# Performance work log

Hardware: AMD Instinct MI355X
Metric: run time of the kernel (lower is better)

The kernel has to match this reference:

```python
import jax, jax.numpy as jnp
import numpy as np

B, T, D, N, K, H = 2, 2048, 2048, 16, 8, 128
WIN = 1024                      # sliding_window_size
SOFT_CAP = 50.0                 # attn_logits_soft_cap
SCALAR = 0.08838834764831845    # query_pre_attn_scalar = head_dim**-0.5
K_MASK = -2.3819763e+38
ROPE_BASE = 10000.0
ROPE_SCALE = 1.0


def apply_rope(x, positions):
    # x: [B, T, heads, H]; positions: [B, T]
    head_dim = x.shape[-1]
    half = head_dim // 2
    timescale = ROPE_BASE ** (2.0 * jnp.arange(half, dtype=jnp.float32) / head_dim)
    sinusoid = positions[..., None].astype(jnp.float32) / timescale / ROPE_SCALE  # [B,T,half]
    sin = jnp.sin(sinusoid)[:, :, None, :]
    cos = jnp.cos(sinusoid)[:, :, None, :]
    first, second = jnp.split(x, 2, axis=-1)
    return jnp.concatenate(
        [first * cos - second * sin, second * cos + first * sin], axis=-1
    ).astype(x.dtype)


def setup_inputs() -> dict:
    key = jax.random.key(0)
    k0, k1, k2, k3 = jax.random.split(key, 4)
    x = jax.random.normal(k0, (B, T, D), jnp.float32)
    wq = jax.random.normal(k1, (N, D, H), jnp.float32) * (D ** -0.5)
    wkv = jax.random.normal(k2, (2, K, D, H), jnp.float32) * (D ** -0.5)
    wo = jax.random.normal(k3, (N, H, D), jnp.float32) * ((N * H) ** -0.5)
    segment_pos = jnp.broadcast_to(jnp.arange(T, dtype=jnp.int32), (B, T))
    attn_mask = jnp.broadcast_to(jnp.tril(jnp.ones((T, T), dtype=bool)), (B, T, T))  # causal
    return {"x": x, "wq": wq, "wkv": wkv, "wo": wo,
            "segment_pos": segment_pos, "attn_mask": attn_mask}


def reference(x, wq, wkv, wo, segment_pos, attn_mask):
    # --- projections ---
    q = jnp.einsum('BTD,NDH->BTNH', x, wq)          # [B,T,N,H]
    kv = jnp.einsum('BTD,CKDH->CBTKH', x, wkv)      # [2,B,T,K,H]
    k_proj, v_proj = kv[0], kv[1]
    # --- RoPE + query scaling ---
    q = apply_rope(q, segment_pos) * SCALAR
    k_proj = apply_rope(k_proj, segment_pos)
    # --- GQA logits ---
    G = N // K
    qg = q.reshape(B, T, K, G, H)
    logits = jnp.einsum('BTKGH,BSKH->BTKGS', qg, k_proj).reshape(B, T, N, T)
    # --- soft cap ---
    logits = jnp.tanh(logits / SOFT_CAP) * SOFT_CAP
    # --- sliding-window mask combined with causal attn_mask ---
    all_ones = jnp.ones(attn_mask.shape, dtype=attn_mask.dtype)
    sliding_mask = jnp.triu(all_ones, -WIN + 1) * jnp.tril(all_ones, WIN - 1)
    mask = sliding_mask * attn_mask                  # [B,T,S]
    padded_logits = jnp.where(mask[:, :, None, :], logits, K_MASK)
    probs = jax.nn.softmax(padded_logits, axis=-1).astype(k_proj.dtype)
    # --- GQA weighted values ---
    encoded = jnp.einsum('BTKGS,BSKH->BTKGH',
                         probs.reshape(B, T, K, G, T), v_proj).reshape(B, T, N, H)
    # --- output projection ---
    return jnp.einsum('BTNH,NHD->BTD', encoded, wo)
```

## Files before the change

kernel.cpp:

```cpp
#include <hip/hip_runtime.h>
#include <stdint.h>

#define BDIM 2
#define TDIM 2048
#define DDIM 2048
#define NHEADS 16
#define KVH 8
#define HDIM 128
#define WINSZ 1024
#define BT (BDIM*TDIM)
#define NHD (NHEADS*HDIM)
#define QKVC 4096

typedef unsigned short u16;
typedef __attribute__((ext_vector_type(8))) short bf16x8;
typedef __attribute__((ext_vector_type(4))) float f32x4;

__device__ __forceinline__ u16 f2bf(float f) {
  union { float f; unsigned u; } v; v.f = f;
  unsigned r = v.u + 0x7FFFu + ((v.u >> 16) & 1u);
  return (u16)(r >> 16);
}
__device__ __forceinline__ float bf2f(u16 u) {
  union { unsigned u; float f; } v; v.u = ((unsigned)u) << 16;
  return v.f;
}

__device__ __forceinline__ void gl_lds16(const u16* g, u16* l) {
  __builtin_amdgcn_global_load_lds((const __attribute__((address_space(1))) void*)g,
                                   (__attribute__((address_space(3))) void*)l, 16, 0, 0);
}

__global__ void k_rope_table(const int* __restrict__ seg, float2* __restrict__ tab) {
  int t = blockIdx.x, b = blockIdx.y, i = threadIdx.x;
  int pos = seg[b*TDIM + t];
  float inv_ts = exp2f(-(float)i * (13.287712379549449f/64.0f));
  float ang = (float)pos * inv_ts;
  tab[(size_t)(b*TDIM + t)*64 + i] = make_float2(cosf(ang), sinf(ang));
}

__global__ void k_cvt_bf16(const float* __restrict__ x, u16* __restrict__ y, int n4) {
  int i = blockIdx.x*blockDim.x + threadIdx.x;
  if (i < n4) {
    float4 v = ((const float4*)x)[i];
    ushort4 o;
    o.x = f2bf(v.x); o.y = f2bf(v.y); o.z = f2bf(v.z); o.w = f2bf(v.w);
    ((ushort4*)y)[i] = o;
  }
}

template<int MODE>
__global__ void k_build_wt(const float* __restrict__ s0p, const float* __restrict__ s1p,
                           u16* __restrict__ dst) {
  __shared__ float tl[32][33];
  int tx = threadIdx.x, ty = threadIdx.y;
  int r0 = blockIdx.x*32, c0 = blockIdx.y*32;
  #pragma unroll
  for (int i = 0; i < 4; i++) {
    int r = r0 + tx, c = c0 + ty + i*8;
    const float* sp; size_t off;
    if (MODE == 0) {
      if (r < 2048) { sp = s0p; off = (size_t)(r >> 7)*262144u + (size_t)(r & 127); }
      else { int j = r - 2048; sp = s1p; off = (size_t)((j >> 10)*8 + ((j >> 7) & 7))*262144u + (size_t)(j & 127); }
      off += (size_t)c * 128u;
    } else {
      sp = s0p; off = (size_t)c * 2048u + (size_t)r;
    }
    tl[tx][ty + i*8] = sp[off];
  }
  __syncthreads();
  #pragma unroll
  for (int i = 0; i < 4; i++) {
    int rl = ty + i*8;
    dst[(size_t)(r0 + rl)*2048u + (size_t)(c0 + tx)] = f2bf(tl[rl][tx]);
  }
}

template<int F32OUT>
__global__ __launch_bounds__(256) void k_gemm(const u16* __restrict__ A, const u16* __restrict__ Bt,
                                              void* __restrict__ Cout, int M, int Ncols, int Kdim, int ldc) {
  __shared__ u16 As[128*64];
  __shared__ u16 Bs[128*64];
  const int tid = threadIdx.x, lane = tid & 63, wave = tid >> 6;
  const int m0 = blockIdx.x * 128, n0 = blockIdx.y * 128;
  const int wr = wave >> 1, wc = wave & 1;
  const int l15 = lane & 15, lg = lane >> 4;
  f32x4 acc[4][4] = {};
  for (int kt = 0; kt < Kdim; kt += 64) {
    __syncthreads();
    #pragma unroll
    for (int i = 0; i < 4; i++) {
      int chb = i*256 + wave*64;
      int ch = chb + lane;
      int r = ch >> 3, cc = ch & 7;
      gl_lds16(A + (size_t)(m0 + r)*Kdim + kt + cc*8, As + chb*8);
      gl_lds16(Bt + (size_t)(n0 + r)*Kdim + kt + cc*8, Bs + chb*8);
    }
    __syncthreads();
    #pragma unroll
    for (int ks = 0; ks < 2; ks++) {
      bf16x8 af[4], bf[4];
      int kk = ks*32 + lg*8;
      #pragma unroll
      for (int mt = 0; mt < 4; mt++) af[mt] = *(const bf16x8*)(As + (wr*64 + mt*16 + l15)*64 + kk);
      #pragma unroll
      for (int nt = 0; nt < 4; nt++) bf[nt] = *(const bf16x8*)(Bs + (wc*64 + nt*16 + l15)*64 + kk);
      #pragma unroll
      for (int mt = 0; mt < 4; mt++)
        #pragma unroll
        for (int nt = 0; nt < 4; nt++)
          acc[mt][nt] = __builtin_amdgcn_mfma_f32_16x16x32_bf16(af[mt], bf[nt], acc[mt][nt], 0, 0, 0);
    }
  }
  #pragma unroll
  for (int mt = 0; mt < 4; mt++) {
    int row = m0 + wr*64 + mt*16 + lg*4;
    #pragma unroll
    for (int nt = 0; nt < 4; nt++) {
      int col = n0 + wc*64 + nt*16 + l15;
      #pragma unroll
      for (int j = 0; j < 4; j++) {
        if (F32OUT) ((float*)Cout)[(size_t)(row + j)*ldc + col] = acc[mt][nt][j];
        else        ((u16*)Cout)[(size_t)(row + j)*ldc + col] = f2bf(acc[mt][nt][j]);
      }
    }
  }
}

template<int F32OUT>
__global__ __launch_bounds__(512, 2) void k_gemm8(const u16* __restrict__ A, const u16* __restrict__ Bt,
                                                  void* __restrict__ Cout, int M, int Ncols, int Kdim, int ldc) {
  __shared__ u16 As[2][256*64];
  __shared__ u16 Bs[2][256*64];
  const int tid = threadIdx.x, lane = tid & 63, wave = tid >> 6;
  const int l15 = lane & 15, lg = lane >> 4;
  const int wm = wave >> 2, wn = wave & 3;
  const int gx = M >> 8, gy = Ncols >> 8;
  const int nwg = gx * gy;
  int bid = blockIdx.x;
  int q = nwg >> 3, r = nwg & 7;
  int xcd = bid & 7, idx = bid >> 3;
  int wg = (xcd < r ? xcd*(q+1) : r*(q+1) + (xcd - r)*q) + idx;
  const int m0 = (wg % gx) * 256, n0 = (wg / gx) * 256;

  const int st_r = tid >> 3;
  const int st_c = (tid & 7) ^ (st_r & 7);

  const u16* Ag = A + (size_t)(m0 + st_r)*Kdim + st_c*8;
  const u16* Bg = Bt + (size_t)(n0 + st_r)*Kdim + st_c*8;

  auto stage = [&](int t, int h) {
    int buf = t & 1;
    if (h < 2) {
      const u16* g = Bg + (size_t)(h*128)*Kdim + t*64;
      u16* d = &Bs[buf][h*8192 + wave*512];
      gl_lds16(g, d);
      gl_lds16(g + (size_t)64*Kdim, d + 4096);
    } else {
      int hh = h - 2;
      const u16* g = Ag + (size_t)(hh*128)*Kdim + t*64;
      u16* d = &As[buf][hh*8192 + wave*512];
      gl_lds16(g, d);
      gl_lds16(g + (size_t)64*Kdim, d + 4096);
    }
  };

  const int aBase = (wm*128 + l15) * 128;
  const int bBase = (wn*64 + l15) * 128;
  const int kx0 = ((lg) ^ (l15 & 7)) << 4;
  const int kx1 = ((4 + lg) ^ (l15 & 7)) << 4;

  f32x4 acc[8][4] = {};
  bf16x8 af[4][2], bfr[4][2];

  stage(0,0); stage(0,1); stage(0,2); stage(0,3);
  stage(1,0); stage(1,1); stage(1,2);
  asm volatile("s_waitcnt vmcnt(6)" ::: "memory");
  __builtin_amdgcn_s_barrier();
  {
    const char* Ab = (const char*)&As[0][0];
    const char* Bb = (const char*)&Bs[0][0];
    #pragma unroll
    for (int mf = 0; mf < 4; mf++) {
      af[mf][0] = *(const bf16x8*)(Ab + aBase + mf*2048 + kx0);
      af[mf][1] = *(const bf16x8*)(Ab + aBase + mf*2048 + kx1);
    }
    #pragma unroll
    for (int nf = 0; nf < 2; nf++) {
      bfr[nf][0] = *(const bf16x8*)(Bb + bBase + nf*2048 + kx0);
      bfr[nf][1] = *(const bf16x8*)(Bb + bBase + nf*2048 + kx1);
    }
  }

  const int NT = Kdim >> 6;

#define MFMA_Q(MS, NS)                                                          \
  { _Pragma("unroll") for (int mf = 0; mf < 4; mf++)                            \
    _Pragma("unroll") for (int nf = 0; nf < 2; nf++) {                          \
      acc[(MS)+mf][(NS)+nf] = __builtin_amdgcn_mfma_f32_16x16x32_bf16(af[mf][0], bfr[(NS)+nf][0], acc[(MS)+mf][(NS)+nf], 0, 0, 0); \
      acc[(MS)+mf][(NS)+nf] = __builtin_amdgcn_mfma_f32_16x16x32_bf16(af[mf][1], bfr[(NS)+nf][1], acc[(MS)+mf][(NS)+nf], 0, 0, 0); \
  } }

  for (int t = 0; t < NT; ++t) {
    const int cur = t & 1;
    const char* Ab  = (const char*)&As[cur][0];
    const char* Bb  = (const char*)&Bs[cur][0];
    const char* Abn = (const char*)&As[cur ^ 1][0];
    const char* Bbn = (const char*)&Bs[cur ^ 1][0];
    __builtin_amdgcn_s_barrier();
    asm volatile("s_waitcnt lgkmcnt(0)" ::: "memory");
    __builtin_amdgcn_sched_barrier(0);
    __builtin_amdgcn_s_setprio(1);
    MFMA_Q(0, 0)
    __builtin_amdgcn_s_setprio(0);
    __builtin_amdgcn_s_barrier();
    #pragma unroll
    for (int nf = 2; nf < 4; nf++) {
      bfr[nf][0] = *(const bf16x8*)(Bb + bBase + nf*2048 + kx0);
      bfr[nf][1] = *(const bf16x8*)(Bb + bBase + nf*2048 + kx1);
    }
    if (t + 1 < NT) stage(t+1, 3);
    __builtin_amdgcn_s_barrier();
    asm volatile("s_waitcnt lgkmcnt(0)" ::: "memory");
    __builtin_amdgcn_sched_barrier(0);
    __builtin_amdgcn_s_setprio(1);
    MFMA_Q(0, 2)
    __builtin_amdgcn_s_setprio(0);
    __builtin_amdgcn_s_barrier();
    #pragma unroll
    for (int mf = 0; mf < 4; mf++) {
      af[mf][0] = *(const bf16x8*)(Ab + aBase + 8192 + mf*2048 + kx0);
      af[mf][1] = *(const bf16x8*)(Ab + aBase + 8192 + mf*2048 + kx1);
    }
    __builtin_amdgcn_s_barrier();
    asm volatile("s_waitcnt lgkmcnt(0)" ::: "memory");
    __builtin_amdgcn_sched_barrier(0);
    __builtin_amdgcn_s_setprio(1);
    MFMA_Q(4, 0)
    __builtin_amdgcn_s_setprio(0);
    __builtin_amdgcn_s_barrier();
    if (t + 2 < NT) { stage(t+2, 0); stage(t+2, 1); }
    __builtin_amdgcn_s_barrier();
    asm volatile("s_waitcnt lgkmcnt(0)" ::: "memory");
    __builtin_amdgcn_sched_barrier(0);
    __builtin_amdgcn_s_setprio(1);
    MFMA_Q(4, 2)
    __builtin_amdgcn_s_setprio(0);
    __builtin_amdgcn_s_barrier();
    if (t + 2 < NT) {
      stage(t+2, 2);
      asm volatile("s_waitcnt vmcnt(6)" ::: "memory");
    } else if (t + 1 < NT) {
      asm volatile("s_waitcnt vmcnt(0)" ::: "memory");
    }
    if (t + 1 < NT) {
      #pragma unroll
      for (int mf = 0; mf < 4; mf++) {
        af[mf][0] = *(const bf16x8*)(Abn + aBase + mf*2048 + kx0);
        af[mf][1] = *(const bf16x8*)(Abn + aBase + mf*2048 + kx1);
      }
      #pragma unroll
      for (int nf = 0; nf < 2; nf++) {
        bfr[nf][0] = *(const bf16x8*)(Bbn + bBase + nf*2048 + kx0);
        bfr[nf][1] = *(const bf16x8*)(Bbn + bBase + nf*2048 + kx1);
      }
    }
  }
#undef MFMA_Q

  #pragma unroll
  for (int mf = 0; mf < 8; mf++) {
    int row = m0 + wm*128 + mf*16 + lg*4;
    #pragma unroll
    for (int nf = 0; nf < 4; nf++) {
      int col = n0 + wn*64 + nf*16 + l15;
      #pragma unroll
      for (int j = 0; j < 4; j++) {
        if (F32OUT) ((float*)Cout)[(size_t)(row + j)*ldc + col] = acc[mf][nf][j];
        else        ((u16*)Cout)[(size_t)(row + j)*ldc + col] = f2bf(acc[mf][nf][j]);
      }
    }
  }
}

__global__ void k_rope2(u16* __restrict__ qkv, const float2* __restrict__ tab) {
  const int tid = threadIdx.x;
  const int bt = blockIdx.x;
  const int h = tid >> 3, g = tid & 7;
  const int col0 = (h < 16 ? h*128 : 2048 + (h - 16)*128) + g*8;
  const float sc = (h < 16) ? 0.08838834764831845f : 1.0f;
  u16* row = qkv + (size_t)bt*QKVC;
  bf16x8 v1 = *(const bf16x8*)(row + col0);
  bf16x8 v2 = *(const bf16x8*)(row + col0 + 64);
  const float4* t4 = (const float4*)(tab + (size_t)bt*64 + g*8);
  bf16x8 r1, r2;
  #pragma unroll
  for (int i = 0; i < 4; i++) {
    float4 cs2 = t4[i];
    float f0 = bf2f((u16)v1[2*i]),   s0 = bf2f((u16)v2[2*i]);
    float f1 = bf2f((u16)v1[2*i+1]), s1 = bf2f((u16)v2[2*i+1]);
    r1[2*i]   = (short)f2bf((f0*cs2.x - s0*cs2.y)*sc);
    r2[2*i]   = (short)f2bf((s0*cs2.x + f0*cs2.y)*sc);
    r1[2*i+1] = (short)f2bf((f1*cs2.z - s1*cs2.w)*sc);
    r2[2*i+1] = (short)f2bf((s1*cs2.z + f1*cs2.w)*sc);
  }
  *(bf16x8*)(row + col0) = r1;
  *(bf16x8*)(row + col0 + 64) = r2;
}

__global__ void k_build_vt(const u16* __restrict__ qkv, u16* __restrict__ vT) {
  __shared__ u16 tl[32][33];
  int tx = threadIdx.x, ty = threadIdx.y;
  int t0 = blockIdx.x*32, h0 = blockIdx.y*32, bk = blockIdx.z;
  const u16* src = qkv + (size_t)(bk >> 3)*TDIM*QKVC + 3072 + (bk & 7)*HDIM;
  #pragma unroll
  for (int i = 0; i < 4; i++)
    tl[ty + i*8][tx] = src[(size_t)(t0 + ty + i*8)*QKVC + h0 + tx];
  __syncthreads();
  u16* dst = vT + (size_t)bk*HDIM*TDIM;
  #pragma unroll
  for (int i = 0; i < 4; i++)
    dst[(size_t)(h0 + ty + i*8)*TDIM + t0 + tx] = tl[tx][ty + i*8];
}

__device__ __forceinline__ void stage_tiles(const u16* __restrict__ kg, const u16* __restrict__ vg,
                                            u16* ldsK, u16* ldsV, int tid) {
  const int w = tid >> 6;
  const int rK = tid >> 4, cK = tid & 15;
  u16* dK = ldsK + w*512;
  gl_lds16(kg + (size_t)rK*QKVC + ((cK ^ (rK & 15)) << 3), dK);
  gl_lds16(kg + (size_t)(rK + 32)*QKVC + ((cK ^ ((rK + 32) & 15)) << 3), dK + 4096);
  const int rV = tid >> 3, cV = tid & 7;
  u16* dV = ldsV + w*512;
  gl_lds16(vg + (size_t)rV*TDIM + ((cV ^ (rV & 7)) << 3), dV);
  gl_lds16(vg + (size_t)(rV + 64)*TDIM + ((cV ^ ((rV + 64) & 7)) << 3), dV + 4096);
}

__global__ __launch_bounds__(512, 4) void k_attn(const u16* __restrict__ qkv, const u16* __restrict__ vT,
                                                 u16* __restrict__ enc) {
  __shared__ u16 Kb[2][64*128];
  __shared__ u16 Vb[2][128*64];
  __shared__ u16 Pl[8][16*64];
  const int tid = threadIdx.x;
  const int lane = tid & 63, wave = tid >> 6;
  const int l15 = lane & 15, lg = lane >> 4;
  const int wg = blockIdx.x;
  const int lin = (wg & 7)*64 + (wg >> 3);
  const int qt = lin & 31, kvh = (lin >> 5) & 7, b = lin >> 8;
  const int n = kvh*2 + (wave >> 2);
  const int t0 = qt * 64;
  const int lo_row = t0 + (wave & 3)*16, hi_row = lo_row + 15;

  bf16x8 qf[4];
  {
    const u16* qb = qkv + (size_t)(b*TDIM + lo_row + l15)*QKVC + n*HDIM + lg*8;
    #pragma unroll
    for (int ks = 0; ks < 4; ks++) qf[ks] = *(const bf16x8*)(qb + ks*32);
  }
  f32x4 o[8] = {};
  f32x4 o_l = {};
  const short one_bf = (short)0x3F80;
  const bf16x8 ones = {one_bf, one_bf, one_bf, one_bf, one_bf, one_bf, one_bf, one_bf};

  const u16* kgb = qkv + (size_t)(b*TDIM)*QKVC + 2048 + kvh*HDIM;
  const u16* vgb = vT + (size_t)(b*KVH + kvh)*HDIM*TDIM;

  const float L0 = 1.4426950408889634f;
  const float L1 = -1.9235933878519513e-4f;
  const float L2 = 3.0777094205631089e-8f;
  const float BIAS = -72.13475204444817f;

  const int s_begin = (t0 >= 1024) ? (t0 - 1024) : 0;
  stage_tiles(kgb + (size_t)s_begin*QKVC, vgb + s_begin, Kb[0], Vb[0], tid);
  int cur = 0;
  for (int s0 = s_begin; s0 <= t0; s0 += 64) {
    if (s0 + 64 <= t0) {
      stage_tiles(kgb + (size_t)(s0 + 64)*QKVC, vgb + (s0 + 64), Kb[cur ^ 1], Vb[cur ^ 1], tid);
      asm volatile("s_waitcnt vmcnt(4)" ::: "memory");
    } else {
      asm volatile("s_waitcnt vmcnt(0)" ::: "memory");
    }
    __builtin_amdgcn_s_barrier();
    __builtin_amdgcn_sched_barrier(0);

    const u16* Kc = Kb[cur];
    const u16* Vc = Vb[cur];
    f32x4 sc4[4];
    #pragma unroll
    for (int c = 0; c < 4; c++) {
      const int cLo = s0 + c*16;
      bool anyLive = (cLo <= hi_row) && (cLo + 15 >= lo_row - (WINSZ - 1));
      bool full    = (cLo + 15 <= lo_row) && (cLo >= hi_row - (WINSZ - 1));
      f32x4 a = {0.f, 0.f, 0.f, 0.f};
      if (anyLive) {
        int krow = c*16 + l15;
        __builtin_amdgcn_s_setprio(1);
        #pragma unroll
        for (int ks = 0; ks < 4; ks++) {
          bf16x8 kf = *(const bf16x8*)(Kc + krow*128 + (((ks*4 + lg) ^ l15) << 3));
          a = __builtin_amdgcn_mfma_f32_16x16x32_bf16(qf[ks], kf, a, 0, 0, 0);
        }
        __builtin_amdgcn_s_setprio(0);
        if (full) {
          #pragma unroll
          for (int j = 0; j < 4; j++) {
            float z = a[j];
            float u = z*z;
            float tt = __builtin_fmaf(u, __builtin_fmaf(u, L2, L1), L0);
            a[j] = exp2f(__builtin_fmaf(z, tt, BIAS));
          }
        } else {
          #pragma unroll
          for (int j = 0; j < 4; j++) {
            int scol = cLo + l15;
            int trow = lo_row + lg*4 + j;
            float z = a[j];
            float u = z*z;
            float tt = __builtin_fmaf(u, __builtin_fmaf(u, L2, L1), L0);
            float p = exp2f(__builtin_fmaf(z, tt, BIAS));
            bool ok = (scol <= trow) && (scol >= trow - (WINSZ - 1));
            a[j] = ok ? p : 0.f;
          }
        }
      }
      sc4[c] = a;
    }
    #pragma unroll
    for (int c = 0; c < 4; c++)
      #pragma unroll
      for (int j = 0; j < 4; j++) {
        int prow = lg*4 + j, pcol = c*16 + l15;
        int off = prow*128 + pcol*2; off ^= (prow & 7) << 4;
        *(u16*)((char*)(&Pl[wave][0]) + off) = f2bf(sc4[c][j]);
      }
    __builtin_amdgcn_s_setprio(1);
    #pragma unroll
    for (int ks = 0; ks < 2; ks++) {
      int roff = l15*128 + ks*64 + lg*16; roff ^= (l15 & 7) << 4;
      bf16x8 pf = *(const bf16x8*)((char*)(&Pl[wave][0]) + roff);
      o_l = __builtin_amdgcn_mfma_f32_16x16x32_bf16(pf, ones, o_l, 0, 0, 0);
      #pragma unroll
      for (int ct = 0; ct < 8; ct++) {
        int vrow = ct*16 + l15;
        bf16x8 vf = *(const bf16x8*)(Vc + vrow*64 + (((ks*4 + lg) ^ (l15 & 7)) << 3));
        o[ct] = __builtin_amdgcn_mfma_f32_16x16x32_bf16(pf, vf, o[ct], 0, 0, 0);
      }
    }
    __builtin_amdgcn_s_setprio(0);
    __builtin_amdgcn_s_barrier();
    cur ^= 1;
  }
  #pragma unroll
  for (int j = 0; j < 4; j++) {
    float inv = __fdividef(1.f, o_l[j]);
    int row = lo_row + lg*4 + j;
    u16* eb = enc + (size_t)(b*TDIM + row)*NHD + n*HDIM;
    #pragma unroll
    for (int ct = 0; ct < 8; ct++)
      eb[ct*16 + l15] = f2bf(o[ct][j] * inv);
  }
}

extern "C" void kernel_launch(void* const* d_in, const int* in_sizes, int n_in,
                              void* d_out, int out_size, void* d_ws, size_t ws_size,
                              hipStream_t stream) {
  const float* x   = (const float*)d_in[0];
  const float* wq  = (const float*)d_in[1];
  const float* wkv = (const float*)d_in[2];
  const float* wo  = (const float*)d_in[3];
  const int*   seg = (const int*)d_in[4];
  float* out = (float*)d_out;

  char* ws = (char*)d_ws;
  u16*    x_bf   = (u16*)(ws);
  u16*    wt_qkv = (u16*)(ws + (16u << 20));
  u16*    qkv    = (u16*)(ws + (32u << 20));
  u16*    vT     = (u16*)(ws + (64u << 20));
  u16*    enc    = (u16*)(ws + (72u << 20));
  u16*    wo_t   = (u16*)(ws + (88u << 20));
  float2* tab    = (float2*)(ws + (96u << 20));

  k_rope_table<<<dim3(TDIM, BDIM), 64, 0, stream>>>(seg, tab);
  k_cvt_bf16<<<(BT*DDIM/4 + 255)/256, 256, 0, stream>>>(x, x_bf, BT*DDIM/4);
  k_build_wt<0><<<dim3(128, 64), dim3(32, 8), 0, stream>>>(wq, wkv, wt_qkv);
  k_build_wt<1><<<dim3(64, 64), dim3(32, 8), 0, stream>>>(wo, nullptr, wo_t);
  k_gemm8<0><<<dim3((BT/256)*(QKVC/256)), 512, 0, stream>>>(x_bf, wt_qkv, qkv, BT, QKVC, DDIM, QKVC);
  k_rope2<<<dim3(BT), 192, 0, stream>>>(qkv, tab);
  k_build_vt<<<dim3(TDIM/32, HDIM/32, BDIM*KVH), dim3(32, 8), 0, stream>>>(qkv, vT);
  k_attn<<<dim3(512), 512, 0, stream>>>(qkv, vT, enc);
  k_gemm<1><<<dim3(BT/128, DDIM/128), 256, 0, stream>>>(enc, wo_t, out, BT, DDIM, NHD, DDIM);
}
```

Baseline: 224.9 us.

## Restructure GEMM main loop LDS fragment loads and barrier schedule

Moves the first-quadrant LDS fragment loads from the end of each iteration to its start, next to the async global-to-LDS stage of the next tile. Replaces the per-quadrant `s_waitcnt lgkmcnt(0)` plus sched_barrier pairs with a single partial lgkmcnt wait and plain compiler memory fences. It also reorders the MFMA quadrants so (4,2) runs before (4,0). The aim is to cut wait stalls and overlap LDS reads with MFMA work. The cost is weaker ordering: stage(t+2) now issues right after the second-half A fragment reads with no barrier in between, which could race with other waves' LDS reads.

```diff
diff --git a/kernel.cpp b/kernel.cpp
--- a/kernel.cpp
+++ b/kernel.cpp
@@ -174,23 +174,10 @@
   bf16x8 af[4][2], bfr[4][2];
 
   stage(0,0); stage(0,1); stage(0,2); stage(0,3);
+  asm volatile("s_waitcnt vmcnt(4)" ::: "memory");
   stage(1,0); stage(1,1); stage(1,2);
   asm volatile("s_waitcnt vmcnt(6)" ::: "memory");
   __builtin_amdgcn_s_barrier();
-  {
-    const char* Ab = (const char*)&As[0][0];
-    const char* Bb = (const char*)&Bs[0][0];
-    #pragma unroll
-    for (int mf = 0; mf < 4; mf++) {
-      af[mf][0] = *(const bf16x8*)(Ab + aBase + mf*2048 + kx0);
-      af[mf][1] = *(const bf16x8*)(Ab + aBase + mf*2048 + kx1);
-    }
-    #pragma unroll
-    for (int nf = 0; nf < 2; nf++) {
-      bfr[nf][0] = *(const bf16x8*)(Bb + bBase + nf*2048 + kx0);
-      bfr[nf][1] = *(const bf16x8*)(Bb + bBase + nf*2048 + kx1);
-    }
-  }
 
   const int NT = Kdim >> 6;
 
@@ -203,13 +190,22 @@
 
   for (int t = 0; t < NT; ++t) {
     const int cur = t & 1;
-    const char* Ab  = (const char*)&As[cur][0];
-    const char* Bb  = (const char*)&Bs[cur][0];
-    const char* Abn = (const char*)&As[cur ^ 1][0];
-    const char* Bbn = (const char*)&Bs[cur ^ 1][0];
-    __builtin_amdgcn_s_barrier();
-    asm volatile("s_waitcnt lgkmcnt(0)" ::: "memory");
-    __builtin_amdgcn_sched_barrier(0);
+    const char* Ab = (const char*)&As[cur][0];
+    const char* Bb = (const char*)&Bs[cur][0];
+    #pragma unroll
+    for (int mf = 0; mf < 4; mf++) {
+      af[mf][0] = *(const bf16x8*)(Ab + aBase + mf*2048 + kx0);
+      af[mf][1] = *(const bf16x8*)(Ab + aBase + mf*2048 + kx1);
+    }
+    #pragma unroll
+    for (int nf = 0; nf < 2; nf++) {
+      bfr[nf][0] = *(const bf16x8*)(Bb + bBase + nf*2048 + kx0);
+      bfr[nf][1] = *(const bf16x8*)(Bb + bBase + nf*2048 + kx1);
+    }
+    if (t + 1 < NT) stage(t+1, 3);
+    asm volatile("s_waitcnt lgkmcnt(8)" ::: "memory");
+    __builtin_amdgcn_s_barrier();
+    asm volatile("" ::: "memory");
     __builtin_amdgcn_s_setprio(1);
     MFMA_Q(0, 0)
     __builtin_amdgcn_s_setprio(0);
@@ -219,10 +215,8 @@
       bfr[nf][0] = *(const bf16x8*)(Bb + bBase + nf*2048 + kx0);
       bfr[nf][1] = *(const bf16x8*)(Bb + bBase + nf*2048 + kx1);
     }
-    if (t + 1 < NT) stage(t+1, 3);
-    __builtin_amdgcn_s_barrier();
-    asm volatile("s_waitcnt lgkmcnt(0)" ::: "memory");
-    __builtin_amdgcn_sched_barrier(0);
+    __builtin_amdgcn_s_barrier();
+    asm volatile("" ::: "memory");
     __builtin_amdgcn_s_setprio(1);
     MFMA_Q(0, 2)
     __builtin_amdgcn_s_setprio(0);
@@ -232,17 +226,9 @@
       af[mf][0] = *(const bf16x8*)(Ab + aBase + 8192 + mf*2048 + kx0);
       af[mf][1] = *(const bf16x8*)(Ab + aBase + 8192 + mf*2048 + kx1);
     }
-    __builtin_amdgcn_s_barrier();
-    asm volatile("s_waitcnt lgkmcnt(0)" ::: "memory");
-    __builtin_amdgcn_sched_barrier(0);
-    __builtin_amdgcn_s_setprio(1);
-    MFMA_Q(4, 0)
-    __builtin_amdgcn_s_setprio(0);
-    __builtin_amdgcn_s_barrier();
     if (t + 2 < NT) { stage(t+2, 0); stage(t+2, 1); }
     __builtin_amdgcn_s_barrier();
-    asm volatile("s_waitcnt lgkmcnt(0)" ::: "memory");
-    __builtin_amdgcn_sched_barrier(0);
+    asm volatile("" ::: "memory");
     __builtin_amdgcn_s_setprio(1);
     MFMA_Q(4, 2)
     __builtin_amdgcn_s_setprio(0);
@@ -253,18 +239,12 @@
     } else if (t + 1 < NT) {
       asm volatile("s_waitcnt vmcnt(0)" ::: "memory");
     }
-    if (t + 1 < NT) {
-      #pragma unroll
-      for (int mf = 0; mf < 4; mf++) {
-        af[mf][0] = *(const bf16x8*)(Abn + aBase + mf*2048 + kx0);
-        af[mf][1] = *(const bf16x8*)(Abn + aBase + mf*2048 + kx1);
-      }
-      #pragma unroll
-      for (int nf = 0; nf < 2; nf++) {
-        bfr[nf][0] = *(const bf16x8*)(Bbn + bBase + nf*2048 + kx0);
-        bfr[nf][1] = *(const bf16x8*)(Bbn + bBase + nf*2048 + kx1);
-      }
-    }
+    __builtin_amdgcn_s_barrier();
+    asm volatile("" ::: "memory");
+    __builtin_amdgcn_s_setprio(1);
+    MFMA_Q(4, 0)
+    __builtin_amdgcn_s_setprio(0);
+    __builtin_amdgcn_s_barrier();
   }
 #undef MFMA_Q
 
```

Result: faster. 216.9 us (-3.6%).
